# Performance work log

Hardware: AMD Instinct MI355X
Metric: run time of the kernel (lower is better)

The kernel has to match this reference:

```python
import jax, jax.numpy as jnp
import numpy as np

N_INST = 128
N_NOTES = 88
B = 64
TIME_LEN = 201
FREQ_LEN = 52
F_AFTER = (TIME_LEN - 4) * (FREQ_LEN - 4)  # 197*48 = 9456


def setup_inputs() -> dict:
    key = jax.random.key(0)
    k = jax.random.split(key, 8)
    data = jax.random.normal(k[0], (B, 1, TIME_LEN, FREQ_LEN), dtype=jnp.float32)
    w1 = jax.random.normal(k[1], (N_INST, 1, 3, 3), dtype=jnp.float32) * 0.1
    b1 = jax.random.normal(k[2], (N_INST,), dtype=jnp.float32) * 0.1
    # grouped conv: out=N_INST, in_per_group=1 (groups=N_INST)
    w2 = jax.random.normal(k[3], (N_INST, 1, 3, 3), dtype=jnp.float32) * 0.1
    b2 = jax.random.normal(k[4], (N_INST,), dtype=jnp.float32) * 0.1
    # stacked per-instrument Linear weights: [I, n_notes, F]
    wfc = jax.random.normal(k[5], (N_INST, N_NOTES, F_AFTER), dtype=jnp.float32) * 0.01
    bfc = jax.random.normal(k[6], (N_INST, N_NOTES), dtype=jnp.float32) * 0.01
    return {"data": data, "w1": w1, "b1": b1, "w2": w2, "b2": b2, "wfc": wfc, "bfc": bfc}


def reference(data, w1, b1, w2, b2, wfc, bfc):
    dn = ("NCHW", "OIHW", "NCHW")
    # conv1: 1 -> I channels, VALID 3x3
    x = jax.lax.conv_general_dilated(data, w1, (1, 1), "VALID", dimension_numbers=dn)
    x = jax.nn.relu(x + b1[None, :, None, None])
    # conv2: depthwise (groups = I), VALID 3x3
    x = jax.lax.conv_general_dilated(x, w2, (1, 1), "VALID", dimension_numbers=dn,
                                     feature_group_count=N_INST)
    x = jax.nn.relu(x + b2[None, :, None, None])
    bsz = x.shape[0]
    x = x.reshape(bsz, N_INST, -1)  # [B, I, F]
    # per-instrument Linear, batched as a single einsum (replaces the python loop)
    out = jnp.einsum("bif,inf->bin", x, wfc) + bfc[None]
    return jax.nn.sigmoid(out)
```

## Files before the change

### kernel.cpp

```cpp
#include <hip/hip_runtime.h>
#include <stdint.h>


namespace {
constexpr int kB = 64, kI = 128, kN = 88, kT = 201, kF = 52;
constexpr int kT2 = 197, kF2 = 48;
constexpr int kFTOT = kT2 * kF2;
constexpr int kNH = 44;
constexpr int kLDK = 200;
constexpr int kSLABS = 50;
constexpr int kTHREADS = 384;

typedef float f32x4 __attribute__((ext_vector_type(4)));
typedef __bf16 bf16x8 __attribute__((ext_vector_type(8)));
typedef unsigned short u16x8 __attribute__((ext_vector_type(8)));
typedef unsigned short u16x4 __attribute__((ext_vector_type(4)));

__device__ __forceinline__ unsigned short bf16_rne(float f) {
  unsigned int u = __float_as_uint(f);
  u += 0x7fffu + ((u >> 16) & 1u);
  return (unsigned short)(u >> 16);
}

__device__ __forceinline__ void loadrow(float* d, const float* p) {
  float4 a = *(const float4*)p;
  float4 b = *(const float4*)(p + 4);
  float4 c = *(const float4*)(p + 8);
  d[0] = a.x; d[1] = a.y; d[2] = a.z;  d[3] = a.w;
  d[4] = b.x; d[5] = b.y; d[6] = b.z;  d[7] = b.w;
  d[8] = c.x; d[9] = c.y; d[10] = c.z; d[11] = c.w;
}

__device__ __forceinline__ void c1row(float* o, const float* r0, const float* r1,
                                      const float* r2, const float* w, float bias) {
#pragma unroll
  for (int c = 0; c < 10; ++c) {
    float v = bias;
    v += r0[c] * w[0]; v += r0[c + 1] * w[1]; v += r0[c + 2] * w[2];
    v += r1[c] * w[3]; v += r1[c + 1] * w[4]; v += r1[c + 2] * w[5];
    v += r2[c] * w[6]; v += r2[c + 1] * w[7]; v += r2[c + 2] * w[8];
    o[c] = fmaxf(v, 0.0f);
  }
}
}

__global__ __launch_bounds__(kTHREADS, 2) void fused_conv_fc_kernel(
    const float* __restrict__ data, const float* __restrict__ w1,
    const float* __restrict__ b1, const float* __restrict__ w2,
    const float* __restrict__ b2, const float* __restrict__ wfc,
    const float* __restrict__ bfc, float* __restrict__ out) {
  __shared__ unsigned short Ab[kB * kLDK];
  __shared__ unsigned short Bb[48 * kLDK];

  const int tid = threadIdx.x;
  const int i = blockIdx.x >> 1;
  const int nh = blockIdx.x & 1;
  const int nbase = nh * kNH;

  for (int z = tid; z < 4 * kLDK; z += kTHREADS) Bb[kNH * kLDK + z] = 0;

  float w1r[9], w2r[9];
#pragma unroll
  for (int j = 0; j < 9; ++j) { w1r[j] = w1[i * 9 + j]; w2r[j] = w2[i * 9 + j]; }
  const float b1r = b1[i], b2r = b2[i];

  const int bb = tid / 6;
  const int oc = tid - bb * 6;
  const int fr0 = oc * 8;
  const float* dbase = data + bb * (kT * kF) + fr0;

  float c1[6][10];
  float dA[12], dB[12], dC[12], dD[12];
  float4 W[6];

  loadrow(dC, dbase + 0 * kF);
  loadrow(dD, dbase + 1 * kF);
  loadrow(dA, dbase + 2 * kF);
  loadrow(dB, dbase + 3 * kF);
  c1row(c1[0], dC, dD, dA, w1r, b1r);
  c1row(c1[1], dD, dA, dB, w1r, b1r);

#pragma unroll
  for (int j = 0; j < 6; ++j) {
    int q = tid + kTHREADS * j;
    if (q < kNH * 48) {
      int n = q / 48, k4 = q - n * 48;
      W[j] = *(const float4*)(wfc + (size_t)(i * kN + nbase + n) * kFTOT + k4 * 4);
    } else {
      W[j] = make_float4(0.f, 0.f, 0.f, 0.f);
    }
  }

  const int wv = tid >> 6, ln = tid & 63;
  const int nt = wv % 3, mp = wv / 3;
  const int lc = ln & 15, lq = ln >> 4;
  f32x4 acc0 = {0.f, 0.f, 0.f, 0.f};
  f32x4 acc1 = {0.f, 0.f, 0.f, 0.f};

  for (int s = 0; s < kSLABS; ++s) {
    loadrow(dC, dbase + (4 * s + 4) * kF);
    c1row(c1[2], dA, dB, dC, w1r, b1r);
    if (s < kSLABS - 1) {
      loadrow(dD, dbase + (4 * s + 5) * kF);
      c1row(c1[3], dB, dC, dD, w1r, b1r);
      loadrow(dA, dbase + (4 * s + 6) * kF);
      c1row(c1[4], dC, dD, dA, w1r, b1r);
      loadrow(dB, dbase + (4 * s + 7) * kF);
      c1row(c1[5], dD, dA, dB, w1r, b1r);
    }
#pragma unroll
    for (int tl = 0; tl < 4; ++tl) {
      if (tl == 0 || s < kSLABS - 1) {
        u16x8 o8;
#pragma unroll
        for (int c = 0; c < 8; ++c) {
          float v = b2r;
#pragma unroll
          for (int r = 0; r < 3; ++r) {
            v += c1[tl + r][c] * w2r[3 * r];
            v += c1[tl + r][c + 1] * w2r[3 * r + 1];
            v += c1[tl + r][c + 2] * w2r[3 * r + 2];
          }
          o8[c] = bf16_rne(fmaxf(v, 0.0f));
        }
        *(u16x8*)&Ab[bb * kLDK + tl * 48 + fr0] = o8;
      }
    }
#pragma unroll
    for (int j = 0; j < 6; ++j) {
      int q = tid + kTHREADS * j;
      if (q < kNH * 48) {
        int n = q / 48, k4 = q - n * 48;
        u16x4 o;
        o[0] = bf16_rne(W[j].x); o[1] = bf16_rne(W[j].y);
        o[2] = bf16_rne(W[j].z); o[3] = bf16_rne(W[j].w);
        *(u16x4*)&Bb[n * kLDK + k4 * 4] = o;
      }
    }
    if (s + 1 < kSLABS) {
      const int real4 = (s + 1 == kSLABS - 1) ? 12 : 48;
#pragma unroll
      for (int j = 0; j < 6; ++j) {
        int q = tid + kTHREADS * j;
        int n = q / 48, k4 = q - n * 48;
        if (q < kNH * 48 && k4 < real4) {
          W[j] = *(const float4*)(wfc + (size_t)(i * kN + nbase + n) * kFTOT +
                                  (size_t)(s + 1) * 192 + k4 * 4);
        } else {
          W[j] = make_float4(0.f, 0.f, 0.f, 0.f);
        }
      }
    }
    __syncthreads();
    {
      const unsigned short* Ar0 = &Ab[(mp * 32 + lc) * kLDK];
      const unsigned short* Ar1 = Ar0 + 16 * kLDK;
      const unsigned short* Br = &Bb[(nt * 16 + lc) * kLDK];
      const int kq = lq * 8;
      if (s != kSLABS - 1) {
#pragma unroll
        for (int ks = 0; ks < 6; ++ks) {
          int ko = ks * 32 + kq;
          bf16x8 a0 = *(const bf16x8*)(Ar0 + ko);
          bf16x8 a1 = *(const bf16x8*)(Ar1 + ko);
          bf16x8 bfr = *(const bf16x8*)(Br + ko);
          acc0 = __builtin_amdgcn_mfma_f32_16x16x32_bf16(a0, bfr, acc0, 0, 0, 0);
          acc1 = __builtin_amdgcn_mfma_f32_16x16x32_bf16(a1, bfr, acc1, 0, 0, 0);
        }
      } else {
#pragma unroll
        for (int ks = 0; ks < 2; ++ks) {
          int ko = ks * 32 + kq;
          bf16x8 a0 = *(const bf16x8*)(Ar0 + ko);
          bf16x8 a1 = *(const bf16x8*)(Ar1 + ko);
          bf16x8 bfr = *(const bf16x8*)(Br + ko);
          acc0 = __builtin_amdgcn_mfma_f32_16x16x32_bf16(a0, bfr, acc0, 0, 0, 0);
          acc1 = __builtin_amdgcn_mfma_f32_16x16x32_bf16(a1, bfr, acc1, 0, 0, 0);
        }
      }
    }
    __syncthreads();
    if (s < kSLABS - 1) {
#pragma unroll
      for (int c = 0; c < 10; ++c) { c1[0][c] = c1[4][c]; c1[1][c] = c1[5][c]; }
    }
  }

  const int nl = nt * 16 + lc;
  if (nl < kNH) {
    const int ng = nbase + nl;
    const float bias = bfc[i * kN + ng];
#pragma unroll
    for (int r = 0; r < 4; ++r) {
      int b0 = mp * 32 + lq * 4 + r;
      float v0 = acc0[r] + bias;
      out[(size_t)(b0 * kI + i) * kN + ng] = 1.0f / (1.0f + __expf(-v0));
      float v1 = acc1[r] + bias;
      out[(size_t)((b0 + 16) * kI + i) * kN + ng] = 1.0f / (1.0f + __expf(-v1));
    }
  }
}

extern "C" void kernel_launch(void* const* d_in, const int* in_sizes, int n_in,
                              void* d_out, int out_size, void* d_ws, size_t ws_size,
                              hipStream_t stream) {
  const float* data = (const float*)d_in[0];
  const float* w1 = (const float*)d_in[1];
  const float* b1 = (const float*)d_in[2];
  const float* w2 = (const float*)d_in[3];
  const float* b2 = (const float*)d_in[4];
  const float* wfc = (const float*)d_in[5];
  const float* bfc = (const float*)d_in[6];
  float* out = (float*)d_out;
  fused_conv_fc_kernel<<<dim3(kI * 2), dim3(kTHREADS), 0, stream>>>(
      data, w1, b1, w2, b2, wfc, bfc, out);
}
```

Baseline: 754.2 us.

## Split fused conv+FC into separate conv kernel and double-buffered GEMM kernel

Splits the single fused kernel into two. A conv kernel writes the bf16 conv2 activations to workspace, and the conv work is spread over four row groups per instrument. A separate GEMM kernel then streams activations and FC weights through register-prefetched, double-buffered LDS tiles with a swizzled A layout and one barrier per step. The intent is to stop the conv from being computed twice per instrument (once per N-half) and to overlap loads with MFMA work. The cost is a round trip through global memory for the roughly 77MB activation tensor, plus a fallback to the old fused path when workspace is too small.

```diff
diff --git a/kernel.cpp b/kernel.cpp
--- a/kernel.cpp
+++ b/kernel.cpp
@@ -7,14 +7,19 @@
 constexpr int kT2 = 197, kF2 = 48;
 constexpr int kFTOT = kT2 * kF2;
 constexpr int kNH = 44;
+constexpr int kTHREADS = 384;
+constexpr int kKS = 128;
+constexpr int kNS = 74;
+constexpr int kLDB = 152;
 constexpr int kLDK = 200;
 constexpr int kSLABS = 50;
-constexpr int kTHREADS = 384;
 
 typedef float f32x4 __attribute__((ext_vector_type(4)));
 typedef __bf16 bf16x8 __attribute__((ext_vector_type(8)));
 typedef unsigned short u16x8 __attribute__((ext_vector_type(8)));
 typedef unsigned short u16x4 __attribute__((ext_vector_type(4)));
+
+#define BAR_LGKM() asm volatile("s_waitcnt lgkmcnt(0)\n\ts_barrier" ::: "memory")
 
 __device__ __forceinline__ unsigned short bf16_rne(float f) {
   unsigned int u = __float_as_uint(f);
@@ -44,6 +49,190 @@
 }
 }
 
+namespace {
+__device__ __forceinline__ void conv_step(const float* dbase, int lrow,
+    float* dNew, const float* dP2, const float* dP1,
+    float* c1n, const float* c1x, const float* c1y,
+    unsigned short* xout, int t2,
+    const float* w1r, float b1r, const float* w2r, float b2r) {
+  loadrow(dNew, dbase + lrow * kF);
+  c1row(c1n, dP2, dP1, dNew, w1r, b1r);
+  u16x8 o8;
+#pragma unroll
+  for (int c = 0; c < 8; ++c) {
+    float v = b2r;
+    v += c1x[c] * w2r[0] + c1x[c + 1] * w2r[1] + c1x[c + 2] * w2r[2];
+    v += c1y[c] * w2r[3] + c1y[c + 1] * w2r[4] + c1y[c + 2] * w2r[5];
+    v += c1n[c] * w2r[6] + c1n[c + 1] * w2r[7] + c1n[c + 2] * w2r[8];
+    o8[c] = bf16_rne(fmaxf(v, 0.0f));
+  }
+  *(u16x8*)(xout + (size_t)t2 * kF2) = o8;
+}
+}
+
+__global__ __launch_bounds__(kTHREADS, 3) void conv_kernel(
+    const float* __restrict__ data, const float* __restrict__ w1,
+    const float* __restrict__ b1, const float* __restrict__ w2,
+    const float* __restrict__ b2, unsigned short* __restrict__ x) {
+  const int i = blockIdx.x >> 2, rg = blockIdx.x & 3;
+  const int base = rg * 50;
+  const int ntrip = (rg == 3) ? 15 : 16;
+  const int tid = threadIdx.x;
+  const int bb = tid / 6, oc = tid - bb * 6;
+  const float* dbase = data + bb * (kT * kF) + oc * 8;
+  unsigned short* xout = x + ((size_t)(bb * kI + i)) * kFTOT + oc * 8;
+
+  float w1r[9], w2r[9];
+#pragma unroll
+  for (int j = 0; j < 9; ++j) { w1r[j] = w1[i * 9 + j]; w2r[j] = w2[i * 9 + j]; }
+  const float b1r = b1[i], b2r = b2[i];
+
+  float dA[12], dB[12], dC[12], c1A[10], c1B[10], c1C[10];
+  loadrow(dB, dbase + (base + 0) * kF);
+  loadrow(dC, dbase + (base + 1) * kF);
+  loadrow(dA, dbase + (base + 2) * kF);
+  c1row(c1A, dB, dC, dA, w1r, b1r);
+  loadrow(dB, dbase + (base + 3) * kF);
+  c1row(c1B, dC, dA, dB, w1r, b1r);
+
+  int t2 = base;
+  for (int tt = 0; tt < ntrip; ++tt, t2 += 3) {
+    conv_step(dbase, t2 + 4, dC, dA, dB, c1C, c1A, c1B, xout, t2, w1r, b1r, w2r, b2r);
+    conv_step(dbase, t2 + 5, dA, dB, dC, c1A, c1B, c1C, xout, t2 + 1, w1r, b1r, w2r, b2r);
+    conv_step(dbase, t2 + 6, dB, dC, dA, c1B, c1C, c1A, xout, t2 + 2, w1r, b1r, w2r, b2r);
+  }
+  conv_step(dbase, t2 + 4, dC, dA, dB, c1C, c1A, c1B, xout, t2, w1r, b1r, w2r, b2r);
+  conv_step(dbase, t2 + 5, dA, dB, dC, c1A, c1B, c1C, xout, t2 + 1, w1r, b1r, w2r, b2r);
+}
+
+namespace {
+struct Regs {
+  u16x8 a[3];
+  float4 w[4];
+};
+
+__device__ __forceinline__ void issue_tiles(Regs& R, const unsigned short* x,
+                                            const float* wfc, int i, int nbase,
+                                            int t, int tid) {
+#pragma unroll
+  for (int j = 0; j < 3; ++j) {
+    int q = tid + kTHREADS * j;
+    if (q < 1024) {
+      int b = q >> 4, c = q & 15;
+      int k0 = t * kKS + c * 8;
+      if (k0 < kFTOT) {
+        R.a[j] = *(const u16x8*)(x + ((size_t)(b * kI + i)) * kFTOT + k0);
+      } else {
+        u16x8 z = {0, 0, 0, 0, 0, 0, 0, 0};
+        R.a[j] = z;
+      }
+    }
+  }
+#pragma unroll
+  for (int j = 0; j < 4; ++j) {
+    int q = tid + kTHREADS * j;
+    if (q < kNH * 32) {
+      int n = q >> 5, k4 = q & 31;
+      int k0 = t * kKS + k4 * 4;
+      if (k0 < kFTOT) {
+        R.w[j] = *(const float4*)(wfc + ((size_t)(i * kN + nbase + n)) * kFTOT + k0);
+      } else {
+        R.w[j] = make_float4(0.f, 0.f, 0.f, 0.f);
+      }
+    }
+  }
+}
+
+__device__ __forceinline__ void stage_tiles(const Regs& R, unsigned short* Abuf,
+                                            unsigned short* Bbuf, int tid) {
+#pragma unroll
+  for (int j = 0; j < 3; ++j) {
+    int q = tid + kTHREADS * j;
+    if (q < 1024) {
+      int b = q >> 4, c = q & 15;
+      int slot = c * 64 + ((b + c) & 63);
+      *(u16x8*)(Abuf + slot * 8) = R.a[j];
+    }
+  }
+#pragma unroll
+  for (int j = 0; j < 4; ++j) {
+    int q = tid + kTHREADS * j;
+    if (q < kNH * 32) {
+      int n = q >> 5, k4 = q & 31;
+      u16x4 o;
+      o[0] = bf16_rne(R.w[j].x); o[1] = bf16_rne(R.w[j].y);
+      o[2] = bf16_rne(R.w[j].z); o[3] = bf16_rne(R.w[j].w);
+      *(u16x4*)(Bbuf + n * kLDB + k4 * 4) = o;
+    }
+  }
+}
+}
+
+__global__ __launch_bounds__(kTHREADS, 2) void gemm_kernel(
+    const unsigned short* __restrict__ x, const float* __restrict__ wfc,
+    const float* __restrict__ bfc, float* __restrict__ out) {
+  __shared__ unsigned short A[2][1024 * 8];
+  __shared__ unsigned short Bt[2][48 * kLDB];
+  const int tid = threadIdx.x;
+  const int i = blockIdx.x >> 1, nh = blockIdx.x & 1, nbase = nh * kNH;
+
+  for (int z = tid; z < 4 * kLDB; z += kTHREADS) {
+    Bt[0][kNH * kLDB + z] = 0;
+    Bt[1][kNH * kLDB + z] = 0;
+  }
+
+  Regs R0, R1;
+  issue_tiles(R0, x, wfc, i, nbase, 0, tid);
+  stage_tiles(R0, A[0], Bt[0], tid);
+  issue_tiles(R1, x, wfc, i, nbase, 1, tid);
+
+  const int wv = tid >> 6, ln = tid & 63;
+  const int nt = wv % 3, mp = wv / 3;
+  const int lc = ln & 15, lq = ln >> 4;
+  f32x4 acc0 = {0.f, 0.f, 0.f, 0.f};
+  f32x4 acc1 = {0.f, 0.f, 0.f, 0.f};
+
+  BAR_LGKM();
+
+  auto body = [&](int s, Regs& Rst, Regs& Ris) {
+    const int p = s & 1;
+    if (s + 1 < kNS) stage_tiles(Rst, A[1 - p], Bt[1 - p], tid);
+    if (s + 2 < kNS) issue_tiles(Ris, x, wfc, i, nbase, s + 2, tid);
+    const unsigned short* Ap = A[p];
+    const unsigned short* Bp = &Bt[p][(nt * 16 + lc) * kLDB + lq * 8];
+    const int m0 = mp * 32 + lc;
+#pragma unroll
+    for (int ks = 0; ks < 4; ++ks) {
+      const int c = ks * 4 + lq;
+      bf16x8 a0 = *(const bf16x8*)(Ap + (c * 64 + ((m0 + c) & 63)) * 8);
+      bf16x8 a1 = *(const bf16x8*)(Ap + (c * 64 + ((m0 + 16 + c) & 63)) * 8);
+      bf16x8 bb = *(const bf16x8*)(Bp + ks * 32);
+      acc0 = __builtin_amdgcn_mfma_f32_16x16x32_bf16(a0, bb, acc0, 0, 0, 0);
+      acc1 = __builtin_amdgcn_mfma_f32_16x16x32_bf16(a1, bb, acc1, 0, 0, 0);
+    }
+    BAR_LGKM();
+  };
+
+  for (int s = 0; s < kNS; s += 2) {
+    body(s, R1, R0);
+    body(s + 1, R0, R1);
+  }
+
+  const int nl = nt * 16 + lc;
+  if (nl < kNH) {
+    const int ng = nbase + nl;
+    const float bias = bfc[i * kN + ng];
+#pragma unroll
+    for (int r = 0; r < 4; ++r) {
+      int b0 = mp * 32 + lq * 4 + r;
+      float v0 = acc0[r] + bias;
+      out[(size_t)(b0 * kI + i) * kN + ng] = 1.0f / (1.0f + __expf(-v0));
+      float v1 = acc1[r] + bias;
+      out[(size_t)((b0 + 16) * kI + i) * kN + ng] = 1.0f / (1.0f + __expf(-v1));
+    }
+  }
+}
+
 __global__ __launch_bounds__(kTHREADS, 2) void fused_conv_fc_kernel(
     const float* __restrict__ data, const float* __restrict__ w1,
     const float* __restrict__ b1, const float* __restrict__ w2,
@@ -51,35 +240,28 @@
     const float* __restrict__ bfc, float* __restrict__ out) {
   __shared__ unsigned short Ab[kB * kLDK];
   __shared__ unsigned short Bb[48 * kLDK];
-
   const int tid = threadIdx.x;
   const int i = blockIdx.x >> 1;
   const int nh = blockIdx.x & 1;
   const int nbase = nh * kNH;
-
   for (int z = tid; z < 4 * kLDK; z += kTHREADS) Bb[kNH * kLDK + z] = 0;
-
   float w1r[9], w2r[9];
 #pragma unroll
   for (int j = 0; j < 9; ++j) { w1r[j] = w1[i * 9 + j]; w2r[j] = w2[i * 9 + j]; }
   const float b1r = b1[i], b2r = b2[i];
-
   const int bb = tid / 6;
   const int oc = tid - bb * 6;
   const int fr0 = oc * 8;
   const float* dbase = data + bb * (kT * kF) + fr0;
-
   float c1[6][10];
   float dA[12], dB[12], dC[12], dD[12];
   float4 W[6];
-
   loadrow(dC, dbase + 0 * kF);
   loadrow(dD, dbase + 1 * kF);
   loadrow(dA, dbase + 2 * kF);
   loadrow(dB, dbase + 3 * kF);
   c1row(c1[0], dC, dD, dA, w1r, b1r);
   c1row(c1[1], dD, dA, dB, w1r, b1r);
-
 #pragma unroll
   for (int j = 0; j < 6; ++j) {
     int q = tid + kTHREADS * j;
@@ -90,13 +272,11 @@
       W[j] = make_float4(0.f, 0.f, 0.f, 0.f);
     }
   }
-
   const int wv = tid >> 6, ln = tid & 63;
   const int nt = wv % 3, mp = wv / 3;
   const int lc = ln & 15, lq = ln >> 4;
   f32x4 acc0 = {0.f, 0.f, 0.f, 0.f};
   f32x4 acc1 = {0.f, 0.f, 0.f, 0.f};
-
   for (int s = 0; s < kSLABS; ++s) {
     loadrow(dC, dbase + (4 * s + 4) * kF);
     c1row(c1[2], dA, dB, dC, w1r, b1r);
@@ -157,26 +337,14 @@
       const unsigned short* Ar1 = Ar0 + 16 * kLDK;
       const unsigned short* Br = &Bb[(nt * 16 + lc) * kLDK];
       const int kq = lq * 8;
-      if (s != kSLABS - 1) {
-#pragma unroll
-        for (int ks = 0; ks < 6; ++ks) {
-          int ko = ks * 32 + kq;
-          bf16x8 a0 = *(const bf16x8*)(Ar0 + ko);
-          bf16x8 a1 = *(const bf16x8*)(Ar1 + ko);
-          bf16x8 bfr = *(const bf16x8*)(Br + ko);
-          acc0 = __builtin_amdgcn_mfma_f32_16x16x32_bf16(a0, bfr, acc0, 0, 0, 0);
-          acc1 = __builtin_amdgcn_mfma_f32_16x16x32_bf16(a1, bfr, acc1, 0, 0, 0);
-        }
-      } else {
-#pragma unroll
-        for (int ks = 0; ks < 2; ++ks) {
-          int ko = ks * 32 + kq;
-          bf16x8 a0 = *(const bf16x8*)(Ar0 + ko);
-          bf16x8 a1 = *(const bf16x8*)(Ar1 + ko);
-          bf16x8 bfr = *(const bf16x8*)(Br + ko);
-          acc0 = __builtin_amdgcn_mfma_f32_16x16x32_bf16(a0, bfr, acc0, 0, 0, 0);
-          acc1 = __builtin_amdgcn_mfma_f32_16x16x32_bf16(a1, bfr, acc1, 0, 0, 0);
-        }
+      const int kmax = (s != kSLABS - 1) ? 6 : 2;
+      for (int ks = 0; ks < kmax; ++ks) {
+        int ko = ks * 32 + kq;
+        bf16x8 a0 = *(const bf16x8*)(Ar0 + ko);
+        bf16x8 a1 = *(const bf16x8*)(Ar1 + ko);
+        bf16x8 bfr = *(const bf16x8*)(Br + ko);
+        acc0 = __builtin_amdgcn_mfma_f32_16x16x32_bf16(a0, bfr, acc0, 0, 0, 0);
+        acc1 = __builtin_amdgcn_mfma_f32_16x16x32_bf16(a1, bfr, acc1, 0, 0, 0);
       }
     }
     __syncthreads();
@@ -185,7 +353,6 @@
       for (int c = 0; c < 10; ++c) { c1[0][c] = c1[4][c]; c1[1][c] = c1[5][c]; }
     }
   }
-
   const int nl = nt * 16 + lc;
   if (nl < kNH) {
     const int ng = nbase + nl;
@@ -212,6 +379,13 @@
   const float* wfc = (const float*)d_in[5];
   const float* bfc = (const float*)d_in[6];
   float* out = (float*)d_out;
-  fused_conv_fc_kernel<<<dim3(kI * 2), dim3(kTHREADS), 0, stream>>>(
-      data, w1, b1, w2, b2, wfc, bfc, out);
-}
+  const size_t need = (size_t)kB * kI * kFTOT * 2;
+  if (ws_size >= need) {
+    unsigned short* x = (unsigned short*)d_ws;
+    conv_kernel<<<dim3(kI * 4), dim3(kTHREADS), 0, stream>>>(data, w1, b1, w2, b2, x);
+    gemm_kernel<<<dim3(kI * 2), dim3(kTHREADS), 0, stream>>>(x, wfc, bfc, out);
+  } else {
+    fused_conv_fc_kernel<<<dim3(kI * 2), dim3(kTHREADS), 0, stream>>>(
+        data, w1, b1, w2, b2, wfc, bfc, out);
+  }
+}
```

Measured after the change: 705.1 us. -6.5%, faster.

## Split fused conv+FC into separate conv kernel and split-K MFMA GEMM kernel

Applied to the files above, without the earlier changes.

Breaks the fused kernel apart. A conv kernel writes the bf16 activations to workspace, using 512 blocks that split the time axis into four chunks. A GEMM kernel then streams the fp32 FC weights directly from global memory with nontemporal loads and a three-stage register prefetch. It splits K across four wave groups and reduces them through LDS, which removes the per-slab LDS staging and the two barriers per slab. The cost is an extra ~77MB write and reread of intermediate activations, plus a second launch. The fused path stays as a fallback when the workspace is too small.

```diff
diff --git a/kernel.cpp b/kernel.cpp
--- a/kernel.cpp
+++ b/kernel.cpp
@@ -7,9 +7,12 @@
 constexpr int kT2 = 197, kF2 = 48;
 constexpr int kFTOT = kT2 * kF2;
 constexpr int kNH = 44;
+constexpr int kTHREADS = 384;
+constexpr int kGTHREADS = 768;
+constexpr int kKQ = 2368;
+constexpr int kSTEPS = 74;
 constexpr int kLDK = 200;
 constexpr int kSLABS = 50;
-constexpr int kTHREADS = 384;
 
 typedef float f32x4 __attribute__((ext_vector_type(4)));
 typedef __bf16 bf16x8 __attribute__((ext_vector_type(8)));
@@ -20,6 +23,10 @@
   unsigned int u = __float_as_uint(f);
   u += 0x7fffu + ((u >> 16) & 1u);
   return (unsigned short)(u >> 16);
+}
+
+__device__ __forceinline__ bf16x8 as_bf16x8(u16x8 v) {
+  union { u16x8 u; bf16x8 b; } c; c.u = v; return c.b;
 }
 
 __device__ __forceinline__ void loadrow(float* d, const float* p) {
@@ -44,6 +51,157 @@
 }
 }
 
+namespace {
+__device__ __forceinline__ void conv_step(const float* dbase, int lrow,
+    float* dNew, const float* dP2, const float* dP1,
+    float* c1n, const float* c1x, const float* c1y,
+    unsigned short* xout, int t2,
+    const float* w1r, float b1r, const float* w2r, float b2r) {
+  loadrow(dNew, dbase + lrow * kF);
+  c1row(c1n, dP2, dP1, dNew, w1r, b1r);
+  u16x8 o8;
+#pragma unroll
+  for (int c = 0; c < 8; ++c) {
+    float v = b2r;
+    v += c1x[c] * w2r[0] + c1x[c + 1] * w2r[1] + c1x[c + 2] * w2r[2];
+    v += c1y[c] * w2r[3] + c1y[c + 1] * w2r[4] + c1y[c + 2] * w2r[5];
+    v += c1n[c] * w2r[6] + c1n[c + 1] * w2r[7] + c1n[c + 2] * w2r[8];
+    o8[c] = bf16_rne(fmaxf(v, 0.0f));
+  }
+  *(u16x8*)(xout + (size_t)t2 * kF2) = o8;
+}
+}
+
+__global__ __launch_bounds__(kTHREADS, 3) void conv_kernel(
+    const float* __restrict__ data, const float* __restrict__ w1,
+    const float* __restrict__ b1, const float* __restrict__ w2,
+    const float* __restrict__ b2, unsigned short* __restrict__ x) {
+  const int j = blockIdx.x;
+  const int i = ((j >> 5) << 3) | (j & 7);
+  const int rg = (j >> 3) & 3;
+  const int base = rg * 50;
+  const int ntrip = (rg == 3) ? 15 : 16;
+  const int tid = threadIdx.x;
+  const int bb = tid / 6, oc = tid - bb * 6;
+  const float* dbase = data + bb * (kT * kF) + oc * 8;
+  unsigned short* xout = x + ((size_t)(bb * kI + i)) * kFTOT + oc * 8;
+
+  float w1r[9], w2r[9];
+#pragma unroll
+  for (int jj = 0; jj < 9; ++jj) { w1r[jj] = w1[i * 9 + jj]; w2r[jj] = w2[i * 9 + jj]; }
+  const float b1r = b1[i], b2r = b2[i];
+
+  float dA[12], dB[12], dC[12], c1A[10], c1B[10], c1C[10];
+  loadrow(dB, dbase + (base + 0) * kF);
+  loadrow(dC, dbase + (base + 1) * kF);
+  loadrow(dA, dbase + (base + 2) * kF);
+  c1row(c1A, dB, dC, dA, w1r, b1r);
+  loadrow(dB, dbase + (base + 3) * kF);
+  c1row(c1B, dC, dA, dB, w1r, b1r);
+
+  int t2 = base;
+  for (int tt = 0; tt < ntrip; ++tt, t2 += 3) {
+    conv_step(dbase, t2 + 4, dC, dA, dB, c1C, c1A, c1B, xout, t2, w1r, b1r, w2r, b2r);
+    conv_step(dbase, t2 + 5, dA, dB, dC, c1A, c1B, c1C, xout, t2 + 1, w1r, b1r, w2r, b2r);
+    conv_step(dbase, t2 + 6, dB, dC, dA, c1B, c1C, c1A, xout, t2 + 2, w1r, b1r, w2r, b2r);
+  }
+  conv_step(dbase, t2 + 4, dC, dA, dB, c1C, c1A, c1B, xout, t2, w1r, b1r, w2r, b2r);
+  conv_step(dbase, t2 + 5, dA, dB, dC, c1A, c1B, c1C, xout, t2 + 1, w1r, b1r, w2r, b2r);
+}
+
+__global__ __launch_bounds__(kGTHREADS, 1) void gemm_kernel(
+    const unsigned short* __restrict__ x, const float* __restrict__ wfc,
+    const float* __restrict__ bfc, float* __restrict__ out) {
+  __shared__ f32x4 red[3][3][4][64];
+
+  const int j = blockIdx.x;
+  const int i = ((j >> 4) << 3) | (j & 7);
+  const int nh = (j >> 3) & 1;
+  const int nbase = nh * kNH;
+  const int tid = threadIdx.x;
+  const int wv = tid >> 6, ln = tid & 63;
+  const int nt = wv % 3, kq = wv / 3;
+  const int lc = ln & 15, lq = ln >> 4;
+  const int kqb = kq * kKQ;
+
+  const unsigned short* xr[4];
+#pragma unroll
+  for (int mt = 0; mt < 4; ++mt)
+    xr[mt] = x + ((size_t)((mt * 16 + lc) * kI + i)) * kFTOT;
+  int brow = i * kN + nbase + nt * 16 + lc;
+  if (brow > kI * kN - 1) brow = kI * kN - 1;
+  const float* wr = wfc + (size_t)brow * kFTOT;
+
+  f32x4 acc[4];
+#pragma unroll
+  for (int mt = 0; mt < 4; ++mt) acc[mt] = f32x4{0.f, 0.f, 0.f, 0.f};
+
+  struct Set { u16x8 a[4]; f32x4 w0, w1; };
+  Set S0, S1, S2;
+
+  auto issue = [&](Set& S, int s) {
+    const int k0 = kqb + s * 32 + lq * 8;
+#pragma unroll
+    for (int mt = 0; mt < 4; ++mt) S.a[mt] = *(const u16x8*)(xr[mt] + k0);
+    const f32x4 z = {0.f, 0.f, 0.f, 0.f};
+    S.w0 = (k0 + 4 <= kFTOT) ? __builtin_nontemporal_load((const f32x4*)(wr + k0)) : z;
+    S.w1 = (k0 + 8 <= kFTOT) ? __builtin_nontemporal_load((const f32x4*)(wr + k0 + 4)) : z;
+  };
+  auto consume = [&](Set& S) {
+    u16x8 bb;
+#pragma unroll
+    for (int e = 0; e < 4; ++e) {
+      bb[e] = bf16_rne(S.w0[e]);
+      bb[e + 4] = bf16_rne(S.w1[e]);
+    }
+    bf16x8 bf = as_bf16x8(bb);
+#pragma unroll
+    for (int mt = 0; mt < 4; ++mt)
+      acc[mt] = __builtin_amdgcn_mfma_f32_16x16x32_bf16(as_bf16x8(S.a[mt]), bf,
+                                                        acc[mt], 0, 0, 0);
+  };
+
+  issue(S0, 0); issue(S1, 1); issue(S2, 2);
+  for (int s = 0; s < 72; s += 3) {
+    consume(S0); if (s + 3 < kSTEPS) issue(S0, s + 3);
+    consume(S1); if (s + 4 < kSTEPS) issue(S1, s + 4);
+    consume(S2); if (s + 5 < kSTEPS) issue(S2, s + 5);
+  }
+  consume(S0);
+  consume(S1);
+
+  if (kq != 0) {
+#pragma unroll
+    for (int mt = 0; mt < 4; ++mt) red[nt][kq - 1][mt][ln] = acc[mt];
+  }
+  __syncthreads();
+  if (kq == 0) {
+#pragma unroll
+    for (int mt = 0; mt < 4; ++mt) {
+#pragma unroll
+      for (int q = 0; q < 3; ++q) {
+        f32x4 p = red[nt][q][mt][ln];
+        acc[mt][0] += p[0]; acc[mt][1] += p[1];
+        acc[mt][2] += p[2]; acc[mt][3] += p[3];
+      }
+    }
+    const int nl = nt * 16 + lc;
+    if (nl < kNH) {
+      const int ng = nbase + nl;
+      const float bias = bfc[i * kN + ng];
+#pragma unroll
+      for (int mt = 0; mt < 4; ++mt) {
+#pragma unroll
+        for (int r = 0; r < 4; ++r) {
+          const int b0 = mt * 16 + lq * 4 + r;
+          const float v = acc[mt][r] + bias;
+          out[(size_t)(b0 * kI + i) * kN + ng] = 1.0f / (1.0f + __expf(-v));
+        }
+      }
+    }
+  }
+}
+
 __global__ __launch_bounds__(kTHREADS, 2) void fused_conv_fc_kernel(
     const float* __restrict__ data, const float* __restrict__ w1,
     const float* __restrict__ b1, const float* __restrict__ w2,
@@ -51,52 +209,43 @@
     const float* __restrict__ bfc, float* __restrict__ out) {
   __shared__ unsigned short Ab[kB * kLDK];
   __shared__ unsigned short Bb[48 * kLDK];
-
   const int tid = threadIdx.x;
   const int i = blockIdx.x >> 1;
   const int nh = blockIdx.x & 1;
   const int nbase = nh * kNH;
-
   for (int z = tid; z < 4 * kLDK; z += kTHREADS) Bb[kNH * kLDK + z] = 0;
-
   float w1r[9], w2r[9];
 #pragma unroll
-  for (int j = 0; j < 9; ++j) { w1r[j] = w1[i * 9 + j]; w2r[j] = w2[i * 9 + j]; }
+  for (int jj = 0; jj < 9; ++jj) { w1r[jj] = w1[i * 9 + jj]; w2r[jj] = w2[i * 9 + jj]; }
   const float b1r = b1[i], b2r = b2[i];
-
   const int bb = tid / 6;
   const int oc = tid - bb * 6;
   const int fr0 = oc * 8;
   const float* dbase = data + bb * (kT * kF) + fr0;
-
   float c1[6][10];
   float dA[12], dB[12], dC[12], dD[12];
   float4 W[6];
-
   loadrow(dC, dbase + 0 * kF);
   loadrow(dD, dbase + 1 * kF);
   loadrow(dA, dbase + 2 * kF);
   loadrow(dB, dbase + 3 * kF);
   c1row(c1[0], dC, dD, dA, w1r, b1r);
   c1row(c1[1], dD, dA, dB, w1r, b1r);
-
-#pragma unroll
-  for (int j = 0; j < 6; ++j) {
-    int q = tid + kTHREADS * j;
+#pragma unroll
+  for (int jj = 0; jj < 6; ++jj) {
+    int q = tid + kTHREADS * jj;
     if (q < kNH * 48) {
       int n = q / 48, k4 = q - n * 48;
-      W[j] = *(const float4*)(wfc + (size_t)(i * kN + nbase + n) * kFTOT + k4 * 4);
+      W[jj] = *(const float4*)(wfc + (size_t)(i * kN + nbase + n) * kFTOT + k4 * 4);
     } else {
-      W[j] = make_float4(0.f, 0.f, 0.f, 0.f);
-    }
-  }
-
+      W[jj] = make_float4(0.f, 0.f, 0.f, 0.f);
+    }
+  }
   const int wv = tid >> 6, ln = tid & 63;
   const int nt = wv % 3, mp = wv / 3;
   const int lc = ln & 15, lq = ln >> 4;
   f32x4 acc0 = {0.f, 0.f, 0.f, 0.f};
   f32x4 acc1 = {0.f, 0.f, 0.f, 0.f};
-
   for (int s = 0; s < kSLABS; ++s) {
     loadrow(dC, dbase + (4 * s + 4) * kF);
     c1row(c1[2], dA, dB, dC, w1r, b1r);
@@ -127,27 +276,27 @@
       }
     }
 #pragma unroll
-    for (int j = 0; j < 6; ++j) {
-      int q = tid + kTHREADS * j;
+    for (int jj = 0; jj < 6; ++jj) {
+      int q = tid + kTHREADS * jj;
       if (q < kNH * 48) {
         int n = q / 48, k4 = q - n * 48;
         u16x4 o;
-        o[0] = bf16_rne(W[j].x); o[1] = bf16_rne(W[j].y);
-        o[2] = bf16_rne(W[j].z); o[3] = bf16_rne(W[j].w);
+        o[0] = bf16_rne(W[jj].x); o[1] = bf16_rne(W[jj].y);
+        o[2] = bf16_rne(W[jj].z); o[3] = bf16_rne(W[jj].w);
         *(u16x4*)&Bb[n * kLDK + k4 * 4] = o;
       }
     }
     if (s + 1 < kSLABS) {
       const int real4 = (s + 1 == kSLABS - 1) ? 12 : 48;
 #pragma unroll
-      for (int j = 0; j < 6; ++j) {
-        int q = tid + kTHREADS * j;
+      for (int jj = 0; jj < 6; ++jj) {
+        int q = tid + kTHREADS * jj;
         int n = q / 48, k4 = q - n * 48;
         if (q < kNH * 48 && k4 < real4) {
-          W[j] = *(const float4*)(wfc + (size_t)(i * kN + nbase + n) * kFTOT +
+          W[jj] = *(const float4*)(wfc + (size_t)(i * kN + nbase + n) * kFTOT +
                                   (size_t)(s + 1) * 192 + k4 * 4);
         } else {
-          W[j] = make_float4(0.f, 0.f, 0.f, 0.f);
+          W[jj] = make_float4(0.f, 0.f, 0.f, 0.f);
         }
       }
     }
@@ -156,27 +305,15 @@
       const unsigned short* Ar0 = &Ab[(mp * 32 + lc) * kLDK];
       const unsigned short* Ar1 = Ar0 + 16 * kLDK;
       const unsigned short* Br = &Bb[(nt * 16 + lc) * kLDK];
-      const int kq = lq * 8;
-      if (s != kSLABS - 1) {
-#pragma unroll
-        for (int ks = 0; ks < 6; ++ks) {
-          int ko = ks * 32 + kq;
-          bf16x8 a0 = *(const bf16x8*)(Ar0 + ko);
-          bf16x8 a1 = *(const bf16x8*)(Ar1 + ko);
-          bf16x8 bfr = *(const bf16x8*)(Br + ko);
-          acc0 = __builtin_amdgcn_mfma_f32_16x16x32_bf16(a0, bfr, acc0, 0, 0, 0);
-          acc1 = __builtin_amdgcn_mfma_f32_16x16x32_bf16(a1, bfr, acc1, 0, 0, 0);
-        }
-      } else {
-#pragma unroll
-        for (int ks = 0; ks < 2; ++ks) {
-          int ko = ks * 32 + kq;
-          bf16x8 a0 = *(const bf16x8*)(Ar0 + ko);
-          bf16x8 a1 = *(const bf16x8*)(Ar1 + ko);
-          bf16x8 bfr = *(const bf16x8*)(Br + ko);
-          acc0 = __builtin_amdgcn_mfma_f32_16x16x32_bf16(a0, bfr, acc0, 0, 0, 0);
-          acc1 = __builtin_amdgcn_mfma_f32_16x16x32_bf16(a1, bfr, acc1, 0, 0, 0);
-        }
+      const int kqo = lq * 8;
+      const int kmax = (s != kSLABS - 1) ? 6 : 2;
+      for (int ks = 0; ks < kmax; ++ks) {
+        int ko = ks * 32 + kqo;
+        bf16x8 a0 = *(const bf16x8*)(Ar0 + ko);
+        bf16x8 a1 = *(const bf16x8*)(Ar1 + ko);
+        bf16x8 bfr = *(const bf16x8*)(Br + ko);
+        acc0 = __builtin_amdgcn_mfma_f32_16x16x32_bf16(a0, bfr, acc0, 0, 0, 0);
+        acc1 = __builtin_amdgcn_mfma_f32_16x16x32_bf16(a1, bfr, acc1, 0, 0, 0);
       }
     }
     __syncthreads();
@@ -185,7 +322,6 @@
       for (int c = 0; c < 10; ++c) { c1[0][c] = c1[4][c]; c1[1][c] = c1[5][c]; }
     }
   }
-
   const int nl = nt * 16 + lc;
   if (nl < kNH) {
     const int ng = nbase + nl;
@@ -212,6 +348,13 @@
   const float* wfc = (const float*)d_in[5];
   const float* bfc = (const float*)d_in[6];
   float* out = (float*)d_out;
-  fused_conv_fc_kernel<<<dim3(kI * 2), dim3(kTHREADS), 0, stream>>>(
-      data, w1, b1, w2, b2, wfc, bfc, out);
-}
+  const size_t need = (size_t)kB * kI * kFTOT * 2 + 64;
+  if (ws_size >= need) {
+    unsigned short* x = (unsigned short*)d_ws;
+    conv_kernel<<<dim3(kI * 4), dim3(kTHREADS), 0, stream>>>(data, w1, b1, w2, b2, x);
+    gemm_kernel<<<dim3(kI * 2), dim3(kGTHREADS), 0, stream>>>(x, wfc, bfc, out);
+  } else {
+    fused_conv_fc_kernel<<<dim3(kI * 2), dim3(kTHREADS), 0, stream>>>(
+        data, w1, b1, w2, b2, wfc, bfc, out);
+  }
+}
```

Result: slower. 816.5 us (+8.3%).
